# Kernel optimization log

Measured on AMD Instinct MI355X. Metric: run time of the kernel, lower is better.

## Reference

```python
import jax, jax.numpy as jnp
import numpy as np

# module config (matches init_kwargs)
SLICE_W, SLICE_H = 32, 32
STRIDE, WIDTH_INIT = 8, 8
EMBED_DIM = 512
B, H, W = 64, 32, 4096
PAD = (SLICE_W - WIDTH_INIT) // 2  # 12, width padding with constant value 1.0


def setup_inputs() -> dict:
    key = jax.random.key(0)
    k1, k2, k3, k4, k5 = jax.random.split(key, 5)
    u = lambda k, s: jax.random.uniform(k, s, jnp.float32, -0.08, 0.08)
    return {
        "images": jax.random.normal(k1, (B, 1, H, W), jnp.float32),
        "conv_w": u(k2, (1, 1, 3, 3)),          # Conv2d(1,1,3x3) weight (OIHW)
        "conv_b": u(k3, (1,)),
        "lin_w": u(k4, (SLICE_W * SLICE_H, EMBED_DIM)),  # bridge Linear, stored [in,out]
        "lin_b": u(k5, (EMBED_DIM,)),
    }


def reference(images, conv_w, conv_b, lin_w, lin_b):
    b = images.shape[0]
    # pad width with constant 1 (F.pad(..., 'constant', 1))
    padded = jnp.pad(images, ((0, 0), (0, 0), (0, 0), (PAD, PAD)), constant_values=1.0)
    # vectorized replacement of the python loop over stride positions
    starts = np.arange(0, W - 1, STRIDE)               # [S] static
    S = starts.shape[0]                                # 512
    idx = starts[:, None] + np.arange(SLICE_W)[None, :]  # [S, slice_w]
    sl = padded[:, :, :, idx]                          # [B,1,H,S,slice_w]
    sl = jnp.transpose(sl, (0, 3, 1, 2, 4))            # [B,S,1,H,slice_w]
    x = sl.reshape(b * S, 1, H, SLICE_W)               # pixels
    # embedder: Conv2d(1,1,k=3,pad=1) + ReLU
    y = jax.lax.conv_general_dilated(x, conv_w, (1, 1), ((1, 1), (1, 1)))
    y = jax.nn.relu(y + conv_b[None, :, None, None])
    # bridge: Linear(slice_w*slice_h -> embed_dim)
    flat = y.reshape(b * S, H * SLICE_W)
    out = flat @ lin_w + lin_b
    return out.reshape(b, S, EMBED_DIM)
```

## Files before the change

### kernel.cpp

```cpp
#include <hip/hip_runtime.h>
#include <cstdint>
#include <cstddef>

typedef unsigned short u16;
typedef unsigned int   u32;
typedef __attribute__((ext_vector_type(4))) float  f32x4;
typedef __attribute__((ext_vector_type(2))) float  f32x2;
typedef __attribute__((ext_vector_type(2))) u32    u32x2;
typedef __attribute__((ext_vector_type(8))) __bf16 bf16x8;

#define PSW   1056
#define ASTR  72
#define CFW   4128
#define WIN   2080

#define WS_BT  0u
#define WS_CF  1048576u
#define WS_AB  (1048576u + 16908288u)
#define WS_NEED (1048576u + 16908288u + 4194304u)

static __device__ __forceinline__ float b2f(u32 u) {
  union { u32 i; float f; } c; c.i = u << 16; return c.f;
}
static __device__ __forceinline__ u16 f2b(float f) {
  union { float f; u32 i; } c; c.f = f;
  return (u16)((c.i + 0x7FFFu + ((c.i >> 16) & 1u)) >> 16);
}

static __device__ __forceinline__ void gl_lds16(const void* g, void* l) {
  __builtin_amdgcn_global_load_lds(
      (__attribute__((address_space(1))) unsigned int*)(void*)g,
      (__attribute__((address_space(3))) unsigned int*)l, 16, 0, 0);
}
static __device__ __forceinline__ void gl_lds4(const void* g, void* l) {
  __builtin_amdgcn_global_load_lds(
      (__attribute__((address_space(1))) unsigned int*)(void*)g,
      (__attribute__((address_space(3))) unsigned int*)l, 4, 0, 0);
}

__global__ __launch_bounds__(256) void transpose_w(const float* __restrict__ lw,
                                                   u16* __restrict__ bt) {
  __shared__ u16 tile[64][65];
  const int t  = threadIdx.x;
  const int c  = t & 63, r0 = t >> 6;
  const int n0 = blockIdx.x * 64;
  const int k0 = blockIdx.y * 64;
#pragma unroll
  for (int rr = 0; rr < 16; ++rr) {
    const int r = r0 * 16 + rr;
    tile[r][c] = f2b(lw[(size_t)(k0 + r) * 512 + n0 + c]);
  }
  __syncthreads();
#pragma unroll
  for (int rr = 0; rr < 16; ++rr) {
    const int r = r0 * 16 + rr;
    bt[(size_t)(n0 + r) * 1024 + k0 + c] = tile[c][r];
  }
}

__global__ __launch_bounds__(512) void prep2(
    const float* __restrict__ img, const float* __restrict__ cw,
    const float* __restrict__ cb, u16* __restrict__ cf, u32* __restrict__ ab,
    const float* __restrict__ lw, u16* __restrict__ bt)
{
  __shared__ __align__(16) float RING[4 * WIN];
  const int t  = threadIdx.x;
  const int id = blockIdx.x;

  if (id >= 512) {
    u16* tile = (u16*)&RING[0];
    const int c = t & 63, r0 = t >> 6;
    for (int q = 0; q < 16; ++q) {
      const int T  = (id - 512) * 16 + q;
      const int n0 = (T & 7) << 6, k0 = (T >> 3) << 6;
      __syncthreads();
#pragma unroll
      for (int rr = 0; rr < 8; ++rr) {
        const int r = r0 * 8 + rr;
        tile[r * 65 + c] = f2b(lw[(size_t)(k0 + r) * 512 + n0 + c]);
      }
      __syncthreads();
#pragma unroll
      for (int rr = 0; rr < 8; ++rr) {
        const int r = r0 * 8 + rr;
        bt[(size_t)(n0 + r) * 1024 + k0 + c] = tile[c * 65 + r];
      }
    }
    return;
  }

  const int b  = id >> 3, sub = id & 7;
  const int ch = sub & 1, hq = sub >> 1;
  const int h0 = hq << 3;
  const int col0   = ch ? 2032 : 0;
  const int wstart = ch ? 0 : 16;
  const float* imgb = img + (size_t)b * 32 * 4096;

  float w9[9];
#pragma unroll
  for (int q = 0; q < 9; ++q) w9[q] = cw[q];
  const float bias = cb[0];

  auto STAGE = [&](int i) {
    float* sp = RING + (i & 3) * WIN;
    const int hh = h0 - 1 + i;
    if (hh >= 0 && hh <= 31) {
      const float* src = imgb + (ptrdiff_t)hh * 4096 + col0;
      gl_lds16(src + 4 * t, sp + wstart + ((t >> 6) << 8));
      if (t < 4) gl_lds16(src + 2048 + 4 * t, sp + wstart + 2048);
      if (ch == 0) { if (t < 16) sp[t] = (t < 4) ? 0.0f : 1.0f; }
      else         { if (t < 16) sp[2064 + t] = (t < 12) ? 1.0f : 0.0f; }
    } else {
      *(f32x4*)(sp + (t << 2)) = (f32x4)0.0f;
      if (t < 8) *(f32x4*)(sp + 2048 + (t << 2)) = (f32x4)0.0f;
    }
  };

  STAGE(0); STAGE(1); STAGE(2);
  __syncthreads();

#pragma unroll 1
  for (int it = 0; it < 8; ++it) {
    if (it < 7) STAGE(3 + it);
    const int h = h0 + it;
    const float* R0 = RING + (( it      ) & 3) * WIN;
    const float* R1 = RING + ((it + 1) & 3) * WIN;
    const float* R2 = RING + ((it + 2) & 3) * WIN;
    u16* cfrow = cf + (size_t)(b * 32 + h) * CFW;

    f32x4 aa0, aa1, aa2;
    auto CONV4 = [&](int tl, bool exp) {
      const int w4 = tl << 2;
      const f32x4 a0 = *(const f32x4*)(R0 + w4), b0 = *(const f32x4*)(R0 + w4 + 4);
      const float c0 = R0[w4 + 8];
      const f32x4 a1 = *(const f32x4*)(R1 + w4), b1 = *(const f32x4*)(R1 + w4 + 4);
      const float c1 = R1[w4 + 8];
      const f32x4 a2 = *(const f32x4*)(R2 + w4), b2 = *(const f32x4*)(R2 + w4 + 4);
      const float c2 = R2[w4 + 8];
      float o0 = bias, o1 = bias, o2 = bias, o3 = bias;
      o0 += w9[0] * a0.w + w9[1] * b0.x + w9[2] * b0.y;
      o1 += w9[0] * b0.x + w9[1] * b0.y + w9[2] * b0.z;
      o2 += w9[0] * b0.y + w9[1] * b0.z + w9[2] * b0.w;
      o3 += w9[0] * b0.z + w9[1] * b0.w + w9[2] * c0;
      o0 += w9[3] * a1.w + w9[4] * b1.x + w9[5] * b1.y;
      o1 += w9[3] * b1.x + w9[4] * b1.y + w9[5] * b1.z;
      o2 += w9[3] * b1.y + w9[4] * b1.z + w9[5] * b1.w;
      o3 += w9[3] * b1.z + w9[4] * b1.w + w9[5] * c1;
      o0 += w9[6] * a2.w + w9[7] * b2.x + w9[8] * b2.y;
      o1 += w9[6] * b2.x + w9[7] * b2.y + w9[8] * b2.z;
      o2 += w9[6] * b2.y + w9[7] * b2.z + w9[8] * b2.w;
      o3 += w9[6] * b2.z + w9[7] * b2.w + w9[8] * c2;
      u32x2 pk;
      pk.x = (u32)f2b(fmaxf(o0, 0.f)) | ((u32)f2b(fmaxf(o1, 0.f)) << 16);
      pk.y = (u32)f2b(fmaxf(o2, 0.f)) | ((u32)f2b(fmaxf(o3, 0.f)) << 16);
      *(u32x2*)(cfrow + (ch << 11) + (tl << 2)) = pk;
      if (exp) { aa0 = a0; aa1 = a1; aa2 = a2; }
    };

    CONV4(t, true);
    if (ch == 1) {
      if (t < 6) CONV4(512 + t, false);
      if (t == 0) { u32x2 z; z.x = 0u; z.y = 0u; *(u32x2*)(cfrow + 4120) = z; }
    }

    u16* abh = (u16*)ab + (size_t)(b * 32 + h) * 1024;
    if (t & 1) {
      const int j = t >> 1;
      float v = bias;
      v += w9[1] * aa0.x + w9[2] * aa0.y;
      v += w9[4] * aa1.x + w9[5] * aa1.y;
      v += w9[7] * aa2.x + w9[8] * aa2.y;
      abh[((ch << 8) + j) << 1] = f2b(fmaxf(v, 0.f));
    } else if (t >= 8) {
      const int j = (t - 8) >> 1;
      float v = bias;
      v += w9[0] * aa0.z + w9[1] * aa0.w;
      v += w9[3] * aa1.z + w9[4] * aa1.w;
      v += w9[6] * aa2.z + w9[7] * aa2.w;
      abh[(((ch << 8) + j) << 1) | 1] = f2b(fmaxf(v, 0.f));
    } else {
      const int j = 252 + (t >> 1);
      const int wq = 8 * j + 34;
      const f32x2 u0 = *(const f32x2*)(R0 + wq);
      const f32x2 u1 = *(const f32x2*)(R1 + wq);
      const f32x2 u2 = *(const f32x2*)(R2 + wq);
      float v = bias;
      v += w9[0] * u0.x + w9[1] * u0.y;
      v += w9[3] * u1.x + w9[4] * u1.y;
      v += w9[6] * u2.x + w9[7] * u2.y;
      abh[(((ch << 8) + j) << 1) | 1] = f2b(fmaxf(v, 0.f));
    }
    __syncthreads();
  }
}

__global__ __launch_bounds__(256) void gemm_k(
    const u16* __restrict__ cf, const u32* __restrict__ ab,
    const u16* __restrict__ bt, const float* __restrict__ lb,
    float* __restrict__ out)
{
  __shared__ __align__(16) char sm[4224 + 1024 + 16384];
  u16* Ps   = (u16*)sm;
  u32* Ab32 = (u32*)(sm + 4224);
  u16* Bs   = (u16*)(sm + 5248);
  float* Cs = (float*)sm;

  const int t  = threadIdx.x;
  const int orig = blockIdx.y * 4 + blockIdx.x;
  const int wg   = ((orig & 7) << 7) + (orig >> 3);
  const int nt = wg & 3, mt = wg >> 2;
  const int b  = mt >> 2, s0 = (mt & 3) << 7, n0 = nt << 7;
  const int w  = t >> 6, i = t & 63;
  const int wr = w >> 1, wc = w & 1;
  const int lq = i >> 4, lr = i & 15;

  const int cB = (i & 7) ^ ((i >> 3) & 7);
  const u16* btp = bt + (size_t)(n0 + (w << 5) + (i >> 3)) * 1024 + (cB << 3);
  u16* BsW = Bs + (w << 11);

  const int rP  = (t >= 132) ? 1 : 0;
  const int ccP = t - 132 * rP;
  const u16* cfp  = cf + (size_t)(b * 32 + rP) * CFW + (s0 << 3) + (ccP << 3);
  const u16* cfp2 = cf + (size_t)(b * 32 + 1) * CFW + (s0 << 3) + ((124 + t) << 3);
  u16* PsW = Ps + (w << 9);

  const u32* abp = ab + (size_t)(b * 32 + (t >> 7)) * 512 + s0 + (t & 127);
  u32* AbW = Ab32 + (w << 6);

  f32x4 acc[4][4];
#pragma unroll
  for (int a = 0; a < 4; ++a)
#pragma unroll
    for (int c = 0; c < 4; ++c) acc[a][c] = (f32x4)0.0f;

  for (int kk = 0; kk < 16; ++kk) {
    __syncthreads();
    gl_lds16(btp,              BsW);
    gl_lds16(btp +  8 * 1024,  BsW + 512);
    gl_lds16(btp + 16 * 1024,  BsW + 1024);
    gl_lds16(btp + 24 * 1024,  BsW + 1536);
    gl_lds16(cfp, PsW);
    if (t < 8) gl_lds16(cfp2, Ps + 2048);
    gl_lds4(abp, AbW);
    btp += 64; cfp += 2 * CFW; cfp2 += 2 * CFW; abp += 1024;
    __syncthreads();

#pragma unroll
    for (int kc = 0; kc < 2; ++kc) {
      const int bswz = (((kc << 2) + lq) ^ (lr & 7)) << 3;
      bf16x8 af[4], bfv[4];
#pragma unroll
      for (int im = 0; im < 4; ++im) {
        const int ml = wr * 64 + im * 16 + lr;
        af[im] = __builtin_bit_cast(bf16x8,
            *(const uint4*)(Ps + kc * 1056 + ((ml + lq) << 3)));
        const u32 a32 = Ab32[kc * 128 + ml];
        union { u16 u; __bf16 h; } lo, hi;
        lo.u = (u16)(a32 & 0xffffu); hi.u = (u16)(a32 >> 16);
        if (lq == 0) af[im][0] = lo.h;
        if (lq == 3) af[im][7] = hi.h;
      }
#pragma unroll
      for (int jn = 0; jn < 4; ++jn) {
        const int n = wc * 64 + jn * 16 + lr;
        bfv[jn] = __builtin_bit_cast(bf16x8, *(const uint4*)(Bs + (n << 6) + bswz));
      }
#pragma unroll
      for (int im = 0; im < 4; ++im)
#pragma unroll
        for (int jn = 0; jn < 4; ++jn)
          acc[im][jn] = __builtin_amdgcn_mfma_f32_16x16x32_bf16(
              af[im], bfv[jn], acc[im][jn], 0, 0, 0);
    }
  }

  float lbv[4];
#pragma unroll
  for (int jn = 0; jn < 4; ++jn) lbv[jn] = lb[n0 + wc * 64 + jn * 16 + lr];

  const int erow = t >> 3, ecol = (t & 7) << 4;
  const int grow_base = (mt << 7) + ((erow >> 4) * 64) + (erow & 15);

#pragma unroll
  for (int im = 0; im < 4; ++im) {
    __syncthreads();
#pragma unroll
    for (int jn = 0; jn < 4; ++jn) {
      const int cl = wc * 64 + jn * 16 + lr;
#pragma unroll
      for (int r = 0; r < 4; ++r)
        Cs[(wr * 16 + lq * 4 + r) * 132 + cl] = acc[im][jn][r] + lbv[jn];
    }
    __syncthreads();
    const size_t grow = (size_t)(grow_base + im * 16);
    float* orow = out + grow * 512 + n0 + ecol;
    const float* crow = Cs + erow * 132 + ecol;
#pragma unroll
    for (int p = 0; p < 4; ++p)
      *(f32x4*)(orow + p * 4) = *(const f32x4*)(crow + p * 4);
  }
}

__global__ __launch_bounds__(256) void fused_fallback(
    const float* __restrict__ img, const float* __restrict__ cw,
    const float* __restrict__ cb, const u16* __restrict__ bt,
    const float* __restrict__ lb, float* __restrict__ out)
{
  __shared__ __align__(16) u16 Ps[4 * PSW];
  __shared__ __align__(16) u16 As[128 * ASTR];
  __shared__ __align__(16) u16 Bs[128 * ASTR];
  const int t = threadIdx.x, nt = blockIdx.x, mt = blockIdx.y;
  const int b = mt >> 2, s0 = (mt & 3) << 7, X0 = s0 << 3, n0 = nt << 7;
  const float* imgb = img + (size_t)b * 32 * 4096;
  float cwf[9];
#pragma unroll
  for (int q = 0; q < 9; ++q) cwf[q] = cw[q];
  const float bias = cb[0];
  const int wv = t >> 6, l = t & 63;
  const int wr = wv >> 1, wc = wv & 1, lq = l >> 4, lr = l & 15;
  const int sl = t >> 1, hsel = t & 1;
  f32x4 acc[4][4];
#pragma unroll
  for (int a = 0; a < 4; ++a)
#pragma unroll
    for (int c = 0; c < 4; ++c) acc[a][c] = (f32x4)0.0f;
  for (int kk = 0; kk < 16; ++kk) {
    const int h0 = kk << 1;
    __syncthreads();
    uint4 bsv[4];
#pragma unroll
    for (int p = 0; p < 4; ++p) {
      const int idx8 = t + (p << 8);
      const int n = idx8 >> 3, k8 = idx8 & 7;
      bsv[p] = *(const uint4*)(bt + (size_t)(n0 + n) * 1024 + (kk << 6) + (k8 << 3));
    }
    for (int idx = t; idx < 4 * PSW; idx += 256) {
      const int r = idx / PSW, xi = idx - r * PSW;
      const int h = h0 - 1 + r, x = X0 - 1 + xi;
      u16 v = 0;
      if (h >= 0 && h < 32 && x >= 0 && x < 4120)
        v = (x < 12 || x >= 4108) ? (u16)0x3F80 : f2b(imgb[h * 4096 + (x - 12)]);
      Ps[idx] = v;
    }
    __syncthreads();
    {
      const int pbase = (sl << 3);
#pragma unroll
      for (int wb = 0; wb < 32; wb += 16) {
        float o[16];
#pragma unroll
        for (int j = 0; j < 16; ++j) o[j] = bias;
#pragma unroll
        for (int dr = 0; dr < 3; ++dr) {
          const u16* p = Ps + (hsel + dr) * PSW + pbase + wb;
          const uint4 va = *(const uint4*)p;
          const uint4 vb = *(const uint4*)(p + 8);
          const u32   vc = *(const u32*)(p + 16);
          float win[18];
          win[0] = b2f(va.x & 0xffffu); win[1] = b2f(va.x >> 16);
          win[2] = b2f(va.y & 0xffffu); win[3] = b2f(va.y >> 16);
          win[4] = b2f(va.z & 0xffffu); win[5] = b2f(va.z >> 16);
          win[6] = b2f(va.w & 0xffffu); win[7] = b2f(va.w >> 16);
          win[8] = b2f(vb.x & 0xffffu); win[9] = b2f(vb.x >> 16);
          win[10] = b2f(vb.y & 0xffffu); win[11] = b2f(vb.y >> 16);
          win[12] = b2f(vb.z & 0xffffu); win[13] = b2f(vb.z >> 16);
          win[14] = b2f(vb.w & 0xffffu); win[15] = b2f(vb.w >> 16);
          win[16] = b2f(vc & 0xffffu);   win[17] = b2f(vc >> 16);
          if (wb == 0) win[0] = 0.f; else win[17] = 0.f;
          const float w0 = cwf[dr * 3], w1 = cwf[dr * 3 + 1], w2 = cwf[dr * 3 + 2];
#pragma unroll
          for (int j = 0; j < 16; ++j)
            o[j] += w0 * win[j] + w1 * win[j + 1] + w2 * win[j + 2];
        }
        u32 pk[8];
#pragma unroll
        for (int q = 0; q < 8; ++q)
          pk[q] = (u32)f2b(fmaxf(o[2 * q], 0.f)) | ((u32)f2b(fmaxf(o[2 * q + 1], 0.f)) << 16);
        uint4* dst = (uint4*)(As + sl * ASTR + (hsel << 5) + wb);
        dst[0] = make_uint4(pk[0], pk[1], pk[2], pk[3]);
        dst[1] = make_uint4(pk[4], pk[5], pk[6], pk[7]);
      }
    }
#pragma unroll
    for (int p = 0; p < 4; ++p) {
      const int idx8 = t + (p << 8);
      const int n = idx8 >> 3, k8 = idx8 & 7;
      *(uint4*)(Bs + n * ASTR + (k8 << 3)) = bsv[p];
    }
    __syncthreads();
#pragma unroll
    for (int kc = 0; kc < 2; ++kc) {
      const int ko = (kc << 5) + (lq << 3);
      bf16x8 af[4], bfv[4];
#pragma unroll
      for (int im = 0; im < 4; ++im)
        af[im] = __builtin_bit_cast(bf16x8,
            *(const uint4*)(As + (wr * 64 + im * 16 + lr) * ASTR + ko));
#pragma unroll
      for (int jn = 0; jn < 4; ++jn)
        bfv[jn] = __builtin_bit_cast(bf16x8,
            *(const uint4*)(Bs + (wc * 64 + jn * 16 + lr) * ASTR + ko));
#pragma unroll
      for (int im = 0; im < 4; ++im)
#pragma unroll
        for (int jn = 0; jn < 4; ++jn)
          acc[im][jn] = __builtin_amdgcn_mfma_f32_16x16x32_bf16(
              af[im], bfv[jn], acc[im][jn], 0, 0, 0);
    }
  }
#pragma unroll
  for (int jn = 0; jn < 4; ++jn) {
    const int col = n0 + wc * 64 + jn * 16 + lr;
    const float lbv = lb[col];
#pragma unroll
    for (int im = 0; im < 4; ++im) {
      const int row0 = (mt << 7) + wr * 64 + im * 16 + (lq << 2);
#pragma unroll
      for (int r = 0; r < 4; ++r)
        out[(size_t)(row0 + r) * 512 + col] = acc[im][jn][r] + lbv;
    }
  }
}

extern "C" void kernel_launch(void* const* d_in, const int* in_sizes, int n_in,
                              void* d_out, int out_size, void* d_ws, size_t ws_size,
                              hipStream_t stream) {
  const float* img = (const float*)d_in[0];
  const float* cw  = (const float*)d_in[1];
  const float* cb  = (const float*)d_in[2];
  const float* lw  = (const float*)d_in[3];
  const float* lb  = (const float*)d_in[4];
  float* out = (float*)d_out;

  u16* btw = (u16*)((char*)d_ws + WS_BT);

  if (ws_size >= WS_NEED) {
    u16* cfp = (u16*)((char*)d_ws + WS_CF);
    u32* abp = (u32*)((char*)d_ws + WS_AB);
    prep2<<<dim3(520), 512, 0, stream>>>(img, cw, cb, cfp, abp, lw, btw);
    gemm_k<<<dim3(4, 256), 256, 0, stream>>>(cfp, abp, btw, lb, out);
  } else {
    transpose_w<<<dim3(8, 16), 256, 0, stream>>>(lw, btw);
    fused_fallback<<<dim3(4, 256), 256, 0, stream>>>(img, cw, cb, btw, lb, out);
  }
}
```

Before: 161.8 us.

## Merge prep and GEMM into one persistent kernel with a grid-wide barrier

Replaces the two-launch path (prep2 followed by gemm_k) with a single fused_all kernel of 1024 blocks. Each block transposes part of the weights and computes the conv for two image rows, then waits on an atomic-counter grid barrier before running the same MFMA GEMM. The aim is to remove the gap between the two kernel launches and the tail of the prep stage. In exchange it adds a memset launch, a spin barrier that only works if all 1024 blocks are resident at once (launch bounds 256,4), and a simpler prep that reads the convolution inputs directly from global memory instead of staging them through LDS.

Result: slower. 302.1 us (+86.7%).

```diff
diff --git a/kernel.cpp b/kernel.cpp
--- a/kernel.cpp
+++ b/kernel.cpp
@@ -18,6 +18,7 @@
 #define WS_CF  1048576u
 #define WS_AB  (1048576u + 16908288u)
 #define WS_NEED (1048576u + 16908288u + 4194304u)
+#define WS_CTR WS_NEED
 
 static __device__ __forceinline__ float b2f(u32 u) {
   union { u32 i; float f; } c; c.i = u << 16; return c.f;
@@ -38,23 +39,222 @@
       (__attribute__((address_space(3))) unsigned int*)l, 4, 0, 0);
 }
 
-__global__ __launch_bounds__(256) void transpose_w(const float* __restrict__ lw,
-                                                   u16* __restrict__ bt) {
-  __shared__ u16 tile[64][65];
-  const int t  = threadIdx.x;
-  const int c  = t & 63, r0 = t >> 6;
-  const int n0 = blockIdx.x * 64;
-  const int k0 = blockIdx.y * 64;
-#pragma unroll
-  for (int rr = 0; rr < 16; ++rr) {
-    const int r = r0 * 16 + rr;
-    tile[r][c] = f2b(lw[(size_t)(k0 + r) * 512 + n0 + c]);
-  }
+__global__ __launch_bounds__(256, 4) void fused_all(
+    const float* __restrict__ img, const float* __restrict__ cw,
+    const float* __restrict__ cb, const float* __restrict__ lw,
+    const float* __restrict__ lb, float* __restrict__ out,
+    u16* __restrict__ cf, u32* __restrict__ ab, u16* __restrict__ bt,
+    u32* __restrict__ ctr)
+{
+  __shared__ __align__(16) char sm[4224 + 1024 + 16384];
+  const int t    = threadIdx.x;
+  const int orig = blockIdx.x;
+  const int wg   = ((orig & 7) << 7) + (orig >> 3);
+  const int xcd  = wg >> 7, rk = wg & 127;
+
+  {
+    u16* tile = (u16*)sm;
+    const int c = t & 63, r0 = t >> 6;
+    const int n0 = (rk & 7) << 6, k0 = (rk >> 3) << 6;
+#pragma unroll
+    for (int rr = 0; rr < 16; ++rr) {
+      const int r = r0 * 16 + rr;
+      tile[r * 65 + c] = f2b(lw[(size_t)(k0 + r) * 512 + n0 + c]);
+    }
+    __syncthreads();
+#pragma unroll
+    for (int rr = 0; rr < 16; ++rr) {
+      const int r = r0 * 16 + rr;
+      bt[(size_t)(n0 + r) * 1024 + k0 + c] = tile[c * 65 + r];
+    }
+  }
+
+  {
+    const int row2  = rk << 1;
+    const int bb    = (xcd << 3) + (row2 >> 5);
+    const int hbase = row2 & 31;
+    const float* imgb = img + (size_t)bb * 32 * 4096;
+    float w9[9];
+#pragma unroll
+    for (int q = 0; q < 9; ++q) w9[q] = cw[q];
+    const float bias = cb[0];
+
+    for (int hh = hbase; hh < hbase + 2; ++hh) {
+      u16* cfrow = cf + (size_t)(bb * 32 + hh) * CFW;
+
+      auto CONV8 = [&](int c) {
+        float o[8];
+#pragma unroll
+        for (int j = 0; j < 8; ++j) o[j] = bias;
+#pragma unroll
+        for (int dr = 0; dr < 3; ++dr) {
+          const int hr = hh - 1 + dr;
+          if (hr < 0 || hr > 31) continue;
+          const float* rp = imgb + (ptrdiff_t)hr * 4096;
+          float win[16];
+          if (c >= 2 && c < 512) {
+            const f32x4* vp = (const f32x4*)(rp + (c << 3) - 16);
+            *(f32x4*)&win[0]  = vp[0];
+            *(f32x4*)&win[4]  = vp[1];
+            *(f32x4*)&win[8]  = vp[2];
+            *(f32x4*)&win[12] = vp[3];
+          } else {
+#pragma unroll
+            for (int k2 = 0; k2 < 16; ++k2) {
+              const int p  = (c << 3) - 4 + k2;
+              int ci = p - 12; ci = ci < 0 ? 0 : (ci > 4095 ? 4095 : ci);
+              const float v = rp[ci];
+              win[k2] = (p < 12) ? 1.0f : (p >= 4120 ? 0.0f : (p >= 4108 ? 1.0f : v));
+            }
+          }
+          const float w0 = w9[dr * 3], w1 = w9[dr * 3 + 1], w2 = w9[dr * 3 + 2];
+#pragma unroll
+          for (int j = 0; j < 8; ++j)
+            o[j] += w0 * win[j + 3] + w1 * win[j + 4] + w2 * win[j + 5];
+        }
+        u32 pk[4];
+#pragma unroll
+        for (int q = 0; q < 4; ++q)
+          pk[q] = (u32)f2b(fmaxf(o[2 * q], 0.f)) |
+                  ((u32)f2b(fmaxf(o[2 * q + 1], 0.f)) << 16);
+        *(uint4*)(cfrow + (c << 3)) = make_uint4(pk[0], pk[1], pk[2], pk[3]);
+      };
+
+      CONV8(t);
+      CONV8(t + 256);
+      if (t < 3) CONV8(512 + t);
+      if (t == 3) *(uint4*)(cfrow + 4120) = make_uint4(0u, 0u, 0u, 0u);
+
+      u32* abrow = ab + (size_t)(bb * 32 + hh) * 512;
+#pragma unroll
+      for (int ss = 0; ss < 2; ++ss) {
+        const int s = t + (ss << 8);
+        float o0 = bias, o1 = bias;
+#pragma unroll
+        for (int dr = 0; dr < 3; ++dr) {
+          const int hr = hh - 1 + dr;
+          if (hr < 0 || hr > 31) continue;
+          const float* rp = imgb + (ptrdiff_t)hr * 4096;
+          float p0, p1, q0, q1;
+          if (s >= 2)   { f32x2 v = *(const f32x2*)(rp + (s << 3) - 12); p0 = v.x; p1 = v.y; }
+          else          { p0 = 1.0f; p1 = 1.0f; }
+          if (s <= 509) { f32x2 v = *(const f32x2*)(rp + (s << 3) + 18); q0 = v.x; q1 = v.y; }
+          else          { q0 = 1.0f; q1 = 1.0f; }
+          o0 += w9[dr * 3 + 1] * p0 + w9[dr * 3 + 2] * p1;
+          o1 += w9[dr * 3]     * q0 + w9[dr * 3 + 1] * q1;
+        }
+        abrow[s] = (u32)f2b(fmaxf(o0, 0.f)) | ((u32)f2b(fmaxf(o1, 0.f)) << 16);
+      }
+    }
+  }
+
   __syncthreads();
-#pragma unroll
-  for (int rr = 0; rr < 16; ++rr) {
-    const int r = r0 * 16 + rr;
-    bt[(size_t)(n0 + r) * 1024 + k0 + c] = tile[c][r];
+  if (t == 0) {
+    __hip_atomic_fetch_add(ctr, 1u, __ATOMIC_RELEASE, __HIP_MEMORY_SCOPE_AGENT);
+    u32 v;
+    do {
+      __builtin_amdgcn_s_sleep(4);
+      v = __hip_atomic_load(ctr, __ATOMIC_RELAXED, __HIP_MEMORY_SCOPE_AGENT);
+    } while (v < 1024u);
+  }
+  __syncthreads();
+  __threadfence();
+
+  {
+    u16* Ps   = (u16*)sm;
+    u32* Ab32 = (u32*)(sm + 4224);
+    u16* Bs   = (u16*)(sm + 5248);
+    float* Cs = (float*)sm;
+
+    const int nt = wg & 3, mt = wg >> 2;
+    const int b2 = mt >> 2, s0 = (mt & 3) << 7, n0g = nt << 7;
+    const int w  = t >> 6, i = t & 63;
+    const int wr = w >> 1, wc = w & 1;
+    const int lq = i >> 4, lr = i & 15;
+
+    const int cB = (i & 7) ^ ((i >> 3) & 7);
+    const u16* btp = bt + (size_t)(n0g + (w << 5) + (i >> 3)) * 1024 + (cB << 3);
+    u16* BsW = Bs + (w << 11);
+    const int rP  = (t >= 132) ? 1 : 0;
+    const int ccP = t - 132 * rP;
+    const u16* cfp  = cf + (size_t)(b2 * 32 + rP) * CFW + (s0 << 3) + (ccP << 3);
+    const u16* cfp2 = cf + (size_t)(b2 * 32 + 1) * CFW + (s0 << 3) + ((124 + t) << 3);
+    u16* PsW = Ps + (w << 9);
+    const u32* abp = ab + (size_t)(b2 * 32 + (t >> 7)) * 512 + s0 + (t & 127);
+    u32* AbW = Ab32 + (w << 6);
+
+    f32x4 acc[4][4];
+#pragma unroll
+    for (int a = 0; a < 4; ++a)
+#pragma unroll
+      for (int c = 0; c < 4; ++c) acc[a][c] = (f32x4)0.0f;
+
+    for (int kk = 0; kk < 16; ++kk) {
+      __syncthreads();
+      gl_lds16(btp,              BsW);
+      gl_lds16(btp +  8 * 1024,  BsW + 512);
+      gl_lds16(btp + 16 * 1024,  BsW + 1024);
+      gl_lds16(btp + 24 * 1024,  BsW + 1536);
+      gl_lds16(cfp, PsW);
+      if (t < 8) gl_lds16(cfp2, Ps + 2048);
+      gl_lds4(abp, AbW);
+      btp += 64; cfp += 2 * CFW; cfp2 += 2 * CFW; abp += 1024;
+      __syncthreads();
+
+#pragma unroll
+      for (int kc = 0; kc < 2; ++kc) {
+        const int bswz = (((kc << 2) + lq) ^ (lr & 7)) << 3;
+        bf16x8 af[4], bfv[4];
+#pragma unroll
+        for (int im = 0; im < 4; ++im) {
+          const int ml = wr * 64 + im * 16 + lr;
+          af[im] = __builtin_bit_cast(bf16x8,
+              *(const uint4*)(Ps + kc * 1056 + ((ml + lq) << 3)));
+          const u32 a32 = Ab32[kc * 128 + ml];
+          union { u16 u; __bf16 h; } lo, hi;
+          lo.u = (u16)(a32 & 0xffffu); hi.u = (u16)(a32 >> 16);
+          if (lq == 0) af[im][0] = lo.h;
+          if (lq == 3) af[im][7] = hi.h;
+        }
+#pragma unroll
+        for (int jn = 0; jn < 4; ++jn) {
+          const int n = wc * 64 + jn * 16 + lr;
+          bfv[jn] = __builtin_bit_cast(bf16x8, *(const uint4*)(Bs + (n << 6) + bswz));
+        }
+#pragma unroll
+        for (int im = 0; im < 4; ++im)
+#pragma unroll
+          for (int jn = 0; jn < 4; ++jn)
+            acc[im][jn] = __builtin_amdgcn_mfma_f32_16x16x32_bf16(
+                af[im], bfv[jn], acc[im][jn], 0, 0, 0);
+      }
+    }
+
+    float lbv[4];
+#pragma unroll
+    for (int jn = 0; jn < 4; ++jn) lbv[jn] = lb[n0g + wc * 64 + jn * 16 + lr];
+
+    const int erow = t >> 3, ecol = (t & 7) << 4;
+    const int grow_base = (mt << 7) + ((erow >> 4) * 64) + (erow & 15);
+
+#pragma unroll
+    for (int im = 0; im < 4; ++im) {
+      __syncthreads();
+#pragma unroll
+      for (int jn = 0; jn < 4; ++jn) {
+        const int cl = wc * 64 + jn * 16 + lr;
+#pragma unroll
+        for (int r = 0; r < 4; ++r)
+          Cs[(wr * 16 + lq * 4 + r) * 132 + cl] = acc[im][jn][r] + lbv[jn];
+      }
+      __syncthreads();
+      const size_t grow = (size_t)(grow_base + im * 16);
+      float* orow = out + grow * 512 + n0g + ecol;
+      const float* crow = Cs + erow * 132 + ecol;
+#pragma unroll
+      for (int p = 0; p < 4; ++p)
+        *(f32x4*)(orow + p * 4) = *(const f32x4*)(crow + p * 4);
+    }
   }
 }
 
@@ -101,9 +301,9 @@
   for (int q = 0; q < 9; ++q) w9[q] = cw[q];
   const float bias = cb[0];
 
-  auto STAGE = [&](int i) {
-    float* sp = RING + (i & 3) * WIN;
-    const int hh = h0 - 1 + i;
+  auto STAGE = [&](int i2) {
+    float* sp = RING + (i2 & 3) * WIN;
+    const int hh = h0 - 1 + i2;
     if (hh >= 0 && hh <= 31) {
       const float* src = imgb + (ptrdiff_t)hh * 4096 + col0;
       gl_lds16(src + 4 * t, sp + wstart + ((t >> 6) << 8));
@@ -123,7 +323,7 @@
   for (int it = 0; it < 8; ++it) {
     if (it < 7) STAGE(3 + it);
     const int h = h0 + it;
-    const float* R0 = RING + (( it      ) & 3) * WIN;
+    const float* R0 = RING + ((it)     & 3) * WIN;
     const float* R1 = RING + ((it + 1) & 3) * WIN;
     const float* R2 = RING + ((it + 2) & 3) * WIN;
     u16* cfrow = cf + (size_t)(b * 32 + h) * CFW;
@@ -217,13 +417,11 @@
   const int cB = (i & 7) ^ ((i >> 3) & 7);
   const u16* btp = bt + (size_t)(n0 + (w << 5) + (i >> 3)) * 1024 + (cB << 3);
   u16* BsW = Bs + (w << 11);
-
   const int rP  = (t >= 132) ? 1 : 0;
   const int ccP = t - 132 * rP;
   const u16* cfp  = cf + (size_t)(b * 32 + rP) * CFW + (s0 << 3) + (ccP << 3);
   const u16* cfp2 = cf + (size_t)(b * 32 + 1) * CFW + (s0 << 3) + ((124 + t) << 3);
   u16* PsW = Ps + (w << 9);
-
   const u32* abp = ab + (size_t)(b * 32 + (t >> 7)) * 512 + s0 + (t & 127);
   u32* AbW = Ab32 + (w << 6);
 
@@ -298,6 +496,26 @@
 #pragma unroll
     for (int p = 0; p < 4; ++p)
       *(f32x4*)(orow + p * 4) = *(const f32x4*)(crow + p * 4);
+  }
+}
+
+__global__ __launch_bounds__(256) void transpose_w(const float* __restrict__ lw,
+                                                   u16* __restrict__ bt) {
+  __shared__ u16 tile[64][65];
+  const int t  = threadIdx.x;
+  const int c  = t & 63, r0 = t >> 6;
+  const int n0 = blockIdx.x * 64;
+  const int k0 = blockIdx.y * 64;
+#pragma unroll
+  for (int rr = 0; rr < 16; ++rr) {
+    const int r = r0 * 16 + rr;
+    tile[r][c] = f2b(lw[(size_t)(k0 + r) * 512 + n0 + c]);
+  }
+  __syncthreads();
+#pragma unroll
+  for (int rr = 0; rr < 16; ++rr) {
+    const int r = r0 * 16 + rr;
+    bt[(size_t)(n0 + r) * 1024 + k0 + c] = tile[c][r];
   }
 }
 
@@ -434,7 +652,14 @@
 
   u16* btw = (u16*)((char*)d_ws + WS_BT);
 
-  if (ws_size >= WS_NEED) {
+  if (ws_size >= WS_NEED + 4) {
+    u16* cfp = (u16*)((char*)d_ws + WS_CF);
+    u32* abp = (u32*)((char*)d_ws + WS_AB);
+    u32* ctr = (u32*)((char*)d_ws + WS_CTR);
+    hipMemsetAsync(ctr, 0, 4, stream);
+    fused_all<<<dim3(1024), 256, 0, stream>>>(img, cw, cb, lw, lb, out,
+                                              cfp, abp, btw, ctr);
+  } else if (ws_size >= WS_NEED) {
     u16* cfp = (u16*)((char*)d_ws + WS_CF);
     u32* abp = (u32*)((char*)d_ws + WS_AB);
     prep2<<<dim3(520), 512, 0, stream>>>(img, cw, cb, cfp, abp, lw, btw);
```
